# Optimization experiments

Measured on AMD Instinct MI355X. Metric: run time of the kernel, lower is better.

Reference implementation:

```python
import jax, jax.numpy as jnp
import numpy as np

D_MODEL = 1024
NUM_HEADS = 16


def setup_inputs() -> dict:
    key = jax.random.key(0)
    ks = jax.random.split(key, 5)
    B, S, D = 2, 2048, D_MODEL
    scale = 1.0 / np.sqrt(D)
    return {
        "x": jax.random.normal(ks[0], (B, S, D), dtype=jnp.float32),
        "q_proj_weight": jax.random.normal(ks[1], (D, D), dtype=jnp.float32) * scale,
        "k_proj_weight": jax.random.normal(ks[2], (D, D), dtype=jnp.float32) * scale,
        "v_proj_weight": jax.random.normal(ks[3], (D, D), dtype=jnp.float32) * scale,
        "o_proj_weight": jax.random.normal(ks[4], (D, D), dtype=jnp.float32) * scale,
    }


def _attn(x, qw, kw, vw, ow, num_heads):
    B, S, D = x.shape
    d_k = D // num_heads
    q = x @ qw.T  # [B,S,D]
    k = x @ kw.T
    v = x @ vw.T
    # split heads: [B, H, S, d_k]
    q = q.reshape(B, S, num_heads, d_k).transpose(0, 2, 1, 3)
    k = k.reshape(B, S, num_heads, d_k).transpose(0, 2, 1, 3)
    v = v.reshape(B, S, num_heads, d_k).transpose(0, 2, 1, 3)
    scores = jnp.einsum('bhqd,bhkd->bhqk', q, k) / jnp.sqrt(jnp.asarray(d_k, x.dtype))
    causal = jnp.tril(jnp.ones((S, S), dtype=bool))  # [S,S]
    scores = jnp.where(causal[None, None], scores, jnp.asarray(-jnp.inf, x.dtype))
    attn = jax.nn.softmax(scores, axis=-1)
    out = jnp.einsum('bhqk,bhkd->bhqd', attn, v)  # [B,H,S,d_k]
    out = out.transpose(0, 2, 1, 3).reshape(B, S, D)
    return out @ ow.T


def reference(x, q_proj_weight, k_proj_weight, v_proj_weight, o_proj_weight):
    return _attn(x, q_proj_weight, k_proj_weight, v_proj_weight, o_proj_weight, NUM_HEADS)
```

## Files before the change

### kernel.cpp

```cpp
#include <hip/hip_runtime.h>

typedef __attribute__((ext_vector_type(8))) short short8;
typedef __attribute__((ext_vector_type(4))) float f32x4;

#define MFMA(a,b,c) __builtin_amdgcn_mfma_f32_16x16x32_bf16((a),(b),(c),0,0,0)

#define B_  2
#define S_  2048
#define D_  1024
#define H_  16
#define DK  64
#define KDIM 1024

typedef unsigned int u32;
typedef __attribute__((address_space(1))) const u32 gu32;
typedef __attribute__((address_space(3))) u32 lu32;

__device__ __forceinline__ void gll16(const unsigned short* g, unsigned short* l){
  __builtin_amdgcn_global_load_lds((gu32*)g, (lu32*)l, 16, 0, 0);
}

__device__ __forceinline__ unsigned short f2bf(float f){
  unsigned int u = __float_as_uint(f);
  u += 0x7fffu + ((u >> 16) & 1u);
  return (unsigned short)(u >> 16);
}

__device__ __forceinline__ u32 pkbf(float lo, float hi){
  u32 a = __float_as_uint(lo) + 0x8000u;
  u32 b = __float_as_uint(hi) + 0x8000u;
  return __builtin_amdgcn_perm(b, a, 0x07060302u);
}

__global__ void cvt_all(const float* __restrict__ x,  const float* __restrict__ qw,
                        const float* __restrict__ kw, const float* __restrict__ vw,
                        const float* __restrict__ ow,
                        unsigned short* __restrict__ xb,  unsigned short* __restrict__ wqb,
                        unsigned short* __restrict__ wkb, unsigned short* __restrict__ wvb,
                        unsigned short* __restrict__ wob,
                        int n4x, int n4w){
  int i = blockIdx.x * 256 + threadIdx.x;
  const float* src; unsigned short* dst; int n4;
  switch (blockIdx.y) {
    case 0:  src = x;  dst = xb;  n4 = n4x; break;
    case 1:  src = qw; dst = wqb; n4 = n4w; break;
    case 2:  src = kw; dst = wkb; n4 = n4w; break;
    case 3:  src = vw; dst = wvb; n4 = n4w; break;
    default: src = ow; dst = wob; n4 = n4w; break;
  }
  if (i >= n4) return;
  float4 f = reinterpret_cast<const float4*>(src)[i];
  ushort4 u;
  u.x = f2bf(f.x); u.y = f2bf(f.y); u.z = f2bf(f.z); u.w = f2bf(f.w);
  reinterpret_cast<ushort4*>(dst)[i] = u;
}

__global__ __launch_bounds__(256) void gemm_qkv(
    const unsigned short* __restrict__ X,
    const unsigned short* __restrict__ Wq,
    const unsigned short* __restrict__ Wk,
    const unsigned short* __restrict__ Wv,
    unsigned short* __restrict__ Qo,
    unsigned short* __restrict__ Ko,
    unsigned short* __restrict__ Vo)
{
  const int z = blockIdx.z;
  const unsigned short* __restrict__ W = (z == 0) ? Wq : (z == 1) ? Wk : Wv;
  const int n0 = blockIdx.x * 64;
  const int m0 = blockIdx.y * 128;

  __shared__ unsigned short As0[128 * 32];
  __shared__ unsigned short As1[128 * 32];
  __shared__ unsigned short Bs0[64 * 32];
  __shared__ unsigned short Bs1[64 * 32];

  const int tid  = threadIdx.x;
  const int wid  = tid >> 6, lane = tid & 63;
  const int wm   = (wid >> 1) * 64, wn = (wid & 1) * 32;
  const int lr   = lane & 15, lk = (lane >> 4) * 8;

  const int srow = lane >> 2;
  const int scol = (lane & 3) * 8;
  const unsigned short* gA = X + (size_t)(m0 + wid * 32 + srow) * KDIM + scol;
  const unsigned short* gB = W + (size_t)(n0 + wid * 16 + srow) * KDIM + scol;
  unsigned short* lA0 = &As0[(wid * 32) * 32];
  unsigned short* lA1 = &As1[(wid * 32) * 32];
  unsigned short* lB0 = &Bs0[(wid * 16) * 32];
  unsigned short* lB1 = &Bs1[(wid * 16) * 32];

  f32x4 acc[4][2];
  const f32x4 z4 = {0.f, 0.f, 0.f, 0.f};
  for (int i = 0; i < 4; i++)
    for (int j = 0; j < 2; j++) acc[i][j] = z4;

  for (int k0 = 0; k0 < KDIM; k0 += 64) {
    __syncthreads();
    gll16(gA + k0,                  lA0);
    gll16(gA + 16 * KDIM + k0,      lA0 + 16 * 32);
    gll16(gA + k0 + 32,             lA1);
    gll16(gA + 16 * KDIM + k0 + 32, lA1 + 16 * 32);
    gll16(gB + k0,                  lB0);
    gll16(gB + k0 + 32,             lB1);
    __syncthreads();

    short8 a[4], b[2];
    for (int i = 0; i < 4; i++) a[i] = *(const short8*)&As0[(wm + i * 16 + lr) * 32 + lk];
    for (int j = 0; j < 2; j++) b[j] = *(const short8*)&Bs0[(wn + j * 16 + lr) * 32 + lk];
    if (z == 2) {
      for (int i = 0; i < 4; i++)
        for (int j = 0; j < 2; j++)
          acc[i][j] = MFMA(b[j], a[i], acc[i][j]);
    } else {
      for (int i = 0; i < 4; i++)
        for (int j = 0; j < 2; j++)
          acc[i][j] = MFMA(a[i], b[j], acc[i][j]);
    }
    for (int i = 0; i < 4; i++) a[i] = *(const short8*)&As1[(wm + i * 16 + lr) * 32 + lk];
    for (int j = 0; j < 2; j++) b[j] = *(const short8*)&Bs1[(wn + j * 16 + lr) * 32 + lk];
    if (z == 2) {
      for (int i = 0; i < 4; i++)
        for (int j = 0; j < 2; j++)
          acc[i][j] = MFMA(b[j], a[i], acc[i][j]);
    } else {
      for (int i = 0; i < 4; i++)
        for (int j = 0; j < 2; j++)
          acc[i][j] = MFMA(a[i], b[j], acc[i][j]);
    }
  }

  const int rbase = (lane >> 4) * 4;
  if (z == 2) {
    for (int i = 0; i < 4; i++)
      for (int j = 0; j < 2; j++)
        for (int r = 0; r < 4; r++) {
          int dfull = n0 + wn + j * 16 + rbase + r;
          int sfull = m0 + wm + i * 16 + lr;
          int h = dfull >> 6, d = dfull & 63;
          int bb = sfull >> 11, s = sfull & 2047;
          Vo[(((bb * H_ + h) * DK) + d) * S_ + s] = f2bf(acc[i][j][r]);
        }
  } else {
    for (int i = 0; i < 4; i++)
      for (int j = 0; j < 2; j++)
        for (int r = 0; r < 4; r++) {
          int m = m0 + wm + i * 16 + rbase + r;
          int n = n0 + wn + j * 16 + lr;
          float v = acc[i][j][r];
          int bb = m >> 11, s = m & 2047, h = n >> 6, d = n & 63;
          if (z == 0) {
            v *= 0.18033688f;
            Qo[(((bb * H_ + h) * S_) + s) * DK + d] = f2bf(v);
          } else {
            Ko[(((bb * H_ + h) * S_) + s) * DK + d] = f2bf(v);
          }
        }
  }
}

__global__ __launch_bounds__(512, 4) void attn(
    const unsigned short* __restrict__ Q,
    const unsigned short* __restrict__ K,
    const unsigned short* __restrict__ V,
    unsigned short* __restrict__ O)
{
  const int h = blockIdx.y, b = blockIdx.z;
  const int qt = b ? (15 - blockIdx.x) : blockIdx.x;

  const unsigned short* __restrict__ Qh = Q + (size_t)((b * H_ + h) * S_) * DK;
  const unsigned short* __restrict__ Kh = K + (size_t)((b * H_ + h) * S_) * DK;
  const unsigned short* __restrict__ Vh = V + (size_t)((b * H_ + h) * DK) * S_;

  __shared__ unsigned short Ks0[64 * 64];
  __shared__ unsigned short Ks1[64 * 64];
  __shared__ unsigned short Vs0[64 * 64];
  __shared__ unsigned short Vs1[64 * 64];
  __shared__ unsigned short Ps[8][16][72];

  const int tid = threadIdx.x, wid = tid >> 6, lane = tid & 63;
  const int lr = lane & 15;
  const int row4 = (lane >> 4) * 4;
  const int q0 = qt * 128;
  const int qcol = q0 + wid * 16 + lr;
  const int qwmin = q0 + wid * 16;
  const int qwmax = qwmin + 15;
  const int lk = (lane >> 4) * 8;

  const int pc0 = (((lane >> 4) + lr) & 7) * 8;
  const int pc1 = (((lane >> 4) + 4 + lr) & 7) * 8;

  const int sr8 = lane >> 3;
  const int sc8 = lane & 7;
  const int sg  = (sc8 - sr8) & 7;
  const int stRow = wid * 8 + sr8;
  const unsigned short* gK = Kh + (size_t)stRow * DK + sg * 8;
  const unsigned short* gV = Vh + (size_t)stRow * S_ + sg * 8;
  unsigned short* lK0 = &Ks0[wid * 8 * 64];
  unsigned short* lK1 = &Ks1[wid * 8 * 64];
  unsigned short* lV0 = &Vs0[wid * 8 * 64];
  unsigned short* lV1 = &Vs1[wid * 8 * 64];

  const short ONE = (short)0x3F80;
  const short8 ones = {ONE, ONE, ONE, ONE, ONE, ONE, ONE, ONE};

  short8 qf[2];
  qf[0] = *(const short8*)&Qh[(q0 + wid * 16 + lr) * DK + lk];
  qf[1] = *(const short8*)&Qh[(q0 + wid * 16 + lr) * DK + 32 + lk];

  const f32x4 z4 = {0.f, 0.f, 0.f, 0.f};
  f32x4 o[4];
  for (int i = 0; i < 4; i++) o[i] = z4;
  f32x4 rs = z4;

  auto tile = [&](int k0, const unsigned short* KS, const unsigned short* VS){
    if (k0 > qwmax) return;
    f32x4 sc[4];
    for (int nt = 0; nt < 4; nt++) {
      short8 kb0 = *(const short8*)&KS[(nt * 16 + lr) * 64 + pc0];
      short8 kb1 = *(const short8*)&KS[(nt * 16 + lr) * 64 + pc1];
      f32x4 s = MFMA(kb0, qf[0], z4);
      sc[nt] = MFMA(kb1, qf[1], s);
    }
    if (k0 + 63 > qwmin) {
      for (int nt = 0; nt < 4; nt++) {
        int kg = k0 + nt * 16 + row4;
        for (int r = 0; r < 4; r++)
          if (kg + r > qcol) sc[nt][r] = -INFINITY;
      }
    }
    for (int nt = 0; nt < 4; nt++) {
      float p0 = __builtin_amdgcn_exp2f(sc[nt][0]);
      float p1 = __builtin_amdgcn_exp2f(sc[nt][1]);
      float p2 = __builtin_amdgcn_exp2f(sc[nt][2]);
      float p3 = __builtin_amdgcn_exp2f(sc[nt][3]);
      uint2 pk;
      pk.x = pkbf(p0, p1);
      pk.y = pkbf(p2, p3);
      *(uint2*)&Ps[wid][lr][nt * 16 + row4] = pk;
    }
    short8 pf0 = *(const short8*)&Ps[wid][lr][lk];
    short8 pf1 = *(const short8*)&Ps[wid][lr][32 + lk];
    rs = MFMA(ones, pf0, rs);
    rs = MFMA(ones, pf1, rs);
    for (int dt = 0; dt < 4; dt++) {
      short8 vb0 = *(const short8*)&VS[(dt * 16 + lr) * 64 + pc0];
      short8 vb1 = *(const short8*)&VS[(dt * 16 + lr) * 64 + pc1];
      o[dt] = MFMA(vb0, pf0, o[dt]);
      o[dt] = MFMA(vb1, pf1, o[dt]);
    }
  };

  const int kt_end = 2 * qt + 2;

  gll16(gK, lK0);
  gll16(gV, lV0);

  for (int kt = 0; kt < kt_end; kt += 2) {
    const int k0 = kt * 64;
    __syncthreads();
    {
      gll16(gK + (size_t)(k0 + 64) * DK, lK1);
      gll16(gV + (k0 + 64),              lV1);
    }
    tile(k0, Ks0, Vs0);
    __syncthreads();
    if (kt + 2 < kt_end) {
      gll16(gK + (size_t)(k0 + 128) * DK, lK0);
      gll16(gV + (k0 + 128),              lV0);
    }
    tile(k0 + 64, Ks1, Vs1);
  }

  const float inv = 1.0f / rs[0];

  const int srow = q0 + wid * 16 + lr;
  for (int dt = 0; dt < 4; dt++) {
    uint2 pk;
    pk.x = pkbf(o[dt][0] * inv, o[dt][1] * inv);
    pk.y = pkbf(o[dt][2] * inv, o[dt][3] * inv);
    *(uint2*)&O[(size_t)(b * S_ + srow) * D_ + h * DK + dt * 16 + row4] = pk;
  }
}

__global__ __launch_bounds__(256) void gemm_oproj(
    const unsigned short* __restrict__ A,
    const unsigned short* __restrict__ W,
    float* __restrict__ out)
{
  const int n0 = blockIdx.x * 64;
  const int m0 = blockIdx.y * 128;

  __shared__ unsigned short As0[128 * 32];
  __shared__ unsigned short As1[128 * 32];
  __shared__ unsigned short Bs0[64 * 32];
  __shared__ unsigned short Bs1[64 * 32];

  const int tid  = threadIdx.x;
  const int wid  = tid >> 6, lane = tid & 63;
  const int wm   = (wid >> 1) * 64, wn = (wid & 1) * 32;
  const int lr   = lane & 15, lk = (lane >> 4) * 8;

  const int srow = lane >> 2;
  const int scol = (lane & 3) * 8;
  const unsigned short* gA = A + (size_t)(m0 + wid * 32 + srow) * KDIM + scol;
  const unsigned short* gB = W + (size_t)(n0 + wid * 16 + srow) * KDIM + scol;
  unsigned short* lA0 = &As0[(wid * 32) * 32];
  unsigned short* lA1 = &As1[(wid * 32) * 32];
  unsigned short* lB0 = &Bs0[(wid * 16) * 32];
  unsigned short* lB1 = &Bs1[(wid * 16) * 32];

  f32x4 acc[4][2];
  const f32x4 z4 = {0.f, 0.f, 0.f, 0.f};
  for (int i = 0; i < 4; i++)
    for (int j = 0; j < 2; j++) acc[i][j] = z4;

  for (int k0 = 0; k0 < KDIM; k0 += 64) {
    __syncthreads();
    gll16(gA + k0,                  lA0);
    gll16(gA + 16 * KDIM + k0,      lA0 + 16 * 32);
    gll16(gA + k0 + 32,             lA1);
    gll16(gA + 16 * KDIM + k0 + 32, lA1 + 16 * 32);
    gll16(gB + k0,                  lB0);
    gll16(gB + k0 + 32,             lB1);
    __syncthreads();

    short8 a[4], b[2];
    for (int i = 0; i < 4; i++) a[i] = *(const short8*)&As0[(wm + i * 16 + lr) * 32 + lk];
    for (int j = 0; j < 2; j++) b[j] = *(const short8*)&Bs0[(wn + j * 16 + lr) * 32 + lk];
    for (int i = 0; i < 4; i++)
      for (int j = 0; j < 2; j++)
        acc[i][j] = MFMA(a[i], b[j], acc[i][j]);
    for (int i = 0; i < 4; i++) a[i] = *(const short8*)&As1[(wm + i * 16 + lr) * 32 + lk];
    for (int j = 0; j < 2; j++) b[j] = *(const short8*)&Bs1[(wn + j * 16 + lr) * 32 + lk];
    for (int i = 0; i < 4; i++)
      for (int j = 0; j < 2; j++)
        acc[i][j] = MFMA(a[i], b[j], acc[i][j]);
  }

  const int rbase = (lane >> 4) * 4;
  for (int i = 0; i < 4; i++)
    for (int j = 0; j < 2; j++)
      for (int r = 0; r < 4; r++) {
        int m = m0 + wm + i * 16 + rbase + r;
        int n = n0 + wn + j * 16 + lr;
        out[(size_t)m * D_ + n] = acc[i][j][r];
      }
}

extern "C" void kernel_launch(void* const* d_in, const int* in_sizes, int n_in,
                              void* d_out, int out_size, void* d_ws, size_t ws_size,
                              hipStream_t stream) {
  const float* x  = (const float*)d_in[0];
  const float* qw = (const float*)d_in[1];
  const float* kw = (const float*)d_in[2];
  const float* vw = (const float*)d_in[3];
  const float* ow = (const float*)d_in[4];
  float* out = (float*)d_out;

  char* ws = (char*)d_ws;
  size_t off = 0;
  auto alloc = [&](size_t bytes) -> void* {
    void* p = ws + off;
    off += (bytes + 255) & ~(size_t)255;
    return p;
  };
  const size_t XN = (size_t)B_ * S_ * D_;
  const size_t WN = (size_t)D_ * D_;
  unsigned short* xb  = (unsigned short*)alloc(XN * 2);
  unsigned short* wqb = (unsigned short*)alloc(WN * 2);
  unsigned short* wkb = (unsigned short*)alloc(WN * 2);
  unsigned short* wvb = (unsigned short*)alloc(WN * 2);
  unsigned short* wob = (unsigned short*)alloc(WN * 2);
  unsigned short* Qb  = (unsigned short*)alloc(XN * 2);
  unsigned short* Kb  = (unsigned short*)alloc(XN * 2);
  unsigned short* Vb  = (unsigned short*)alloc(XN * 2);
  unsigned short* Ob  = (unsigned short*)alloc(XN * 2);

  cvt_all<<<dim3((XN / 4 + 255) / 256, 5), dim3(256), 0, stream>>>(
      x, qw, kw, vw, ow, xb, wqb, wkb, wvb, wob, (int)(XN / 4), (int)(WN / 4));

  gemm_qkv<<<dim3(D_ / 64, (B_ * S_) / 128, 3), dim3(256), 0, stream>>>(
      xb, wqb, wkb, wvb, Qb, Kb, Vb);

  attn<<<dim3(S_ / 128, H_, B_), dim3(512), 0, stream>>>(Qb, Kb, Vb, Ob);

  gemm_oproj<<<dim3(D_ / 64, (B_ * S_) / 128), dim3(256), 0, stream>>>(Ob, wob, out);
}
```

Before: 171.6 us.

## Enlarge GEMM tiles to 128x128 with XOR-swizzled 64-wide LDS layout

Both projection GEMMs move from 128x64 to 128x128 block tiles, so each wave computes a 64x64 sub-tile (4x4 MFMA accumulators) instead of 64x32. Each K-step of 64 is now stored as one 64-column LDS row with an XOR swizzle on the 16-byte chunk index, replacing the pair of 32-wide buffers, which is meant to avoid LDS bank conflicts. The goal is more MFMA work per LDS load and less global traffic per output. In exchange, accumulator registers double and there are half as many blocks, which may reduce occupancy.

```diff
diff --git a/kernel.cpp b/kernel.cpp
--- a/kernel.cpp
+++ b/kernel.cpp
@@ -66,64 +66,73 @@
 {
   const int z = blockIdx.z;
   const unsigned short* __restrict__ W = (z == 0) ? Wq : (z == 1) ? Wk : Wv;
-  const int n0 = blockIdx.x * 64;
+  const int n0 = blockIdx.x * 128;
   const int m0 = blockIdx.y * 128;
 
-  __shared__ unsigned short As0[128 * 32];
-  __shared__ unsigned short As1[128 * 32];
-  __shared__ unsigned short Bs0[64 * 32];
-  __shared__ unsigned short Bs1[64 * 32];
+  __shared__ unsigned short As[128 * 64];
+  __shared__ unsigned short Bs[128 * 64];
 
   const int tid  = threadIdx.x;
   const int wid  = tid >> 6, lane = tid & 63;
-  const int wm   = (wid >> 1) * 64, wn = (wid & 1) * 32;
-  const int lr   = lane & 15, lk = (lane >> 4) * 8;
-
-  const int srow = lane >> 2;
-  const int scol = (lane & 3) * 8;
+  const int wm   = (wid >> 1) * 64, wn = (wid & 1) * 64;
+  const int lr   = lane & 15, c = lane >> 4;
+  const int sw   = lr & 7;
+  const int pc0  = (c ^ sw) * 8;
+  const int pc1  = ((4 + c) ^ sw) * 8;
+
+  const int srow = lane >> 3;
+  const int scol = ((lane & 7) ^ srow) * 8;
   const unsigned short* gA = X + (size_t)(m0 + wid * 32 + srow) * KDIM + scol;
-  const unsigned short* gB = W + (size_t)(n0 + wid * 16 + srow) * KDIM + scol;
-  unsigned short* lA0 = &As0[(wid * 32) * 32];
-  unsigned short* lA1 = &As1[(wid * 32) * 32];
-  unsigned short* lB0 = &Bs0[(wid * 16) * 32];
-  unsigned short* lB1 = &Bs1[(wid * 16) * 32];
-
-  f32x4 acc[4][2];
+  const unsigned short* gB = W + (size_t)(n0 + wid * 32 + srow) * KDIM + scol;
+  unsigned short* lA = &As[(wid * 32) * 64];
+  unsigned short* lB = &Bs[(wid * 32) * 64];
+
+  f32x4 acc[4][4];
   const f32x4 z4 = {0.f, 0.f, 0.f, 0.f};
   for (int i = 0; i < 4; i++)
-    for (int j = 0; j < 2; j++) acc[i][j] = z4;
+    for (int j = 0; j < 4; j++) acc[i][j] = z4;
 
   for (int k0 = 0; k0 < KDIM; k0 += 64) {
     __syncthreads();
-    gll16(gA + k0,                  lA0);
-    gll16(gA + 16 * KDIM + k0,      lA0 + 16 * 32);
-    gll16(gA + k0 + 32,             lA1);
-    gll16(gA + 16 * KDIM + k0 + 32, lA1 + 16 * 32);
-    gll16(gB + k0,                  lB0);
-    gll16(gB + k0 + 32,             lB1);
-    __syncthreads();
-
-    short8 a[4], b[2];
-    for (int i = 0; i < 4; i++) a[i] = *(const short8*)&As0[(wm + i * 16 + lr) * 32 + lk];
-    for (int j = 0; j < 2; j++) b[j] = *(const short8*)&Bs0[(wn + j * 16 + lr) * 32 + lk];
+#pragma unroll
+    for (int i = 0; i < 4; i++) gll16(gA + (size_t)(i * 8) * KDIM + k0, lA + i * 512);
+#pragma unroll
+    for (int i = 0; i < 4; i++) gll16(gB + (size_t)(i * 8) * KDIM + k0, lB + i * 512);
+    __syncthreads();
+
+    short8 a[4], b[4];
+#pragma unroll
+    for (int i = 0; i < 4; i++) a[i] = *(const short8*)&As[(wm + i * 16 + lr) * 64 + pc0];
+#pragma unroll
+    for (int j = 0; j < 4; j++) b[j] = *(const short8*)&Bs[(wn + j * 16 + lr) * 64 + pc0];
     if (z == 2) {
+#pragma unroll
       for (int i = 0; i < 4; i++)
-        for (int j = 0; j < 2; j++)
+#pragma unroll
+        for (int j = 0; j < 4; j++)
           acc[i][j] = MFMA(b[j], a[i], acc[i][j]);
     } else {
+#pragma unroll
       for (int i = 0; i < 4; i++)
-        for (int j = 0; j < 2; j++)
+#pragma unroll
+        for (int j = 0; j < 4; j++)
           acc[i][j] = MFMA(a[i], b[j], acc[i][j]);
     }
-    for (int i = 0; i < 4; i++) a[i] = *(const short8*)&As1[(wm + i * 16 + lr) * 32 + lk];
-    for (int j = 0; j < 2; j++) b[j] = *(const short8*)&Bs1[(wn + j * 16 + lr) * 32 + lk];
+#pragma unroll
+    for (int i = 0; i < 4; i++) a[i] = *(const short8*)&As[(wm + i * 16 + lr) * 64 + pc1];
+#pragma unroll
+    for (int j = 0; j < 4; j++) b[j] = *(const short8*)&Bs[(wn + j * 16 + lr) * 64 + pc1];
     if (z == 2) {
+#pragma unroll
       for (int i = 0; i < 4; i++)
-        for (int j = 0; j < 2; j++)
+#pragma unroll
+        for (int j = 0; j < 4; j++)
           acc[i][j] = MFMA(b[j], a[i], acc[i][j]);
     } else {
+#pragma unroll
       for (int i = 0; i < 4; i++)
-        for (int j = 0; j < 2; j++)
+#pragma unroll
+        for (int j = 0; j < 4; j++)
           acc[i][j] = MFMA(a[i], b[j], acc[i][j]);
     }
   }
@@ -131,7 +140,7 @@
   const int rbase = (lane >> 4) * 4;
   if (z == 2) {
     for (int i = 0; i < 4; i++)
-      for (int j = 0; j < 2; j++)
+      for (int j = 0; j < 4; j++)
         for (int r = 0; r < 4; r++) {
           int dfull = n0 + wn + j * 16 + rbase + r;
           int sfull = m0 + wm + i * 16 + lr;
@@ -141,7 +150,7 @@
         }
   } else {
     for (int i = 0; i < 4; i++)
-      for (int j = 0; j < 2; j++)
+      for (int j = 0; j < 4; j++)
         for (int r = 0; r < 4; r++) {
           int m = m0 + wm + i * 16 + rbase + r;
           int n = n0 + wn + j * 16 + lr;
@@ -286,59 +295,64 @@
     const unsigned short* __restrict__ W,
     float* __restrict__ out)
 {
-  const int n0 = blockIdx.x * 64;
+  const int n0 = blockIdx.x * 128;
   const int m0 = blockIdx.y * 128;
 
-  __shared__ unsigned short As0[128 * 32];
-  __shared__ unsigned short As1[128 * 32];
-  __shared__ unsigned short Bs0[64 * 32];
-  __shared__ unsigned short Bs1[64 * 32];
+  __shared__ unsigned short As[128 * 64];
+  __shared__ unsigned short Bs[128 * 64];
 
   const int tid  = threadIdx.x;
   const int wid  = tid >> 6, lane = tid & 63;
-  const int wm   = (wid >> 1) * 64, wn = (wid & 1) * 32;
-  const int lr   = lane & 15, lk = (lane >> 4) * 8;
-
-  const int srow = lane >> 2;
-  const int scol = (lane & 3) * 8;
+  const int wm   = (wid >> 1) * 64, wn = (wid & 1) * 64;
+  const int lr   = lane & 15, c = lane >> 4;
+  const int sw   = lr & 7;
+  const int pc0  = (c ^ sw) * 8;
+  const int pc1  = ((4 + c) ^ sw) * 8;
+
+  const int srow = lane >> 3;
+  const int scol = ((lane & 7) ^ srow) * 8;
   const unsigned short* gA = A + (size_t)(m0 + wid * 32 + srow) * KDIM + scol;
-  const unsigned short* gB = W + (size_t)(n0 + wid * 16 + srow) * KDIM + scol;
-  unsigned short* lA0 = &As0[(wid * 32) * 32];
-  unsigned short* lA1 = &As1[(wid * 32) * 32];
-  unsigned short* lB0 = &Bs0[(wid * 16) * 32];
-  unsigned short* lB1 = &Bs1[(wid * 16) * 32];
-
-  f32x4 acc[4][2];
+  const unsigned short* gB = W + (size_t)(n0 + wid * 32 + srow) * KDIM + scol;
+  unsigned short* lA = &As[(wid * 32) * 64];
+  unsigned short* lB = &Bs[(wid * 32) * 64];
+
+  f32x4 acc[4][4];
   const f32x4 z4 = {0.f, 0.f, 0.f, 0.f};
   for (int i = 0; i < 4; i++)
-    for (int j = 0; j < 2; j++) acc[i][j] = z4;
+    for (int j = 0; j < 4; j++) acc[i][j] = z4;
 
   for (int k0 = 0; k0 < KDIM; k0 += 64) {
     __syncthreads();
-    gll16(gA + k0,                  lA0);
-    gll16(gA + 16 * KDIM + k0,      lA0 + 16 * 32);
-    gll16(gA + k0 + 32,             lA1);
-    gll16(gA + 16 * KDIM + k0 + 32, lA1 + 16 * 32);
-    gll16(gB + k0,                  lB0);
-    gll16(gB + k0 + 32,             lB1);
-    __syncthreads();
-
-    short8 a[4], b[2];
-    for (int i = 0; i < 4; i++) a[i] = *(const short8*)&As0[(wm + i * 16 + lr) * 32 + lk];
-    for (int j = 0; j < 2; j++) b[j] = *(const short8*)&Bs0[(wn + j * 16 + lr) * 32 + lk];
+#pragma unroll
+    for (int i = 0; i < 4; i++) gll16(gA + (size_t)(i * 8) * KDIM + k0, lA + i * 512);
+#pragma unroll
+    for (int i = 0; i < 4; i++) gll16(gB + (size_t)(i * 8) * KDIM + k0, lB + i * 512);
+    __syncthreads();
+
+    short8 a[4], b[4];
+#pragma unroll
+    for (int i = 0; i < 4; i++) a[i] = *(const short8*)&As[(wm + i * 16 + lr) * 64 + pc0];
+#pragma unroll
+    for (int j = 0; j < 4; j++) b[j] = *(const short8*)&Bs[(wn + j * 16 + lr) * 64 + pc0];
+#pragma unroll
     for (int i = 0; i < 4; i++)
-      for (int j = 0; j < 2; j++)
+#pragma unroll
+      for (int j = 0; j < 4; j++)
         acc[i][j] = MFMA(a[i], b[j], acc[i][j]);
-    for (int i = 0; i < 4; i++) a[i] = *(const short8*)&As1[(wm + i * 16 + lr) * 32 + lk];
-    for (int j = 0; j < 2; j++) b[j] = *(const short8*)&Bs1[(wn + j * 16 + lr) * 32 + lk];
+#pragma unroll
+    for (int i = 0; i < 4; i++) a[i] = *(const short8*)&As[(wm + i * 16 + lr) * 64 + pc1];
+#pragma unroll
+    for (int j = 0; j < 4; j++) b[j] = *(const short8*)&Bs[(wn + j * 16 + lr) * 64 + pc1];
+#pragma unroll
     for (int i = 0; i < 4; i++)
-      for (int j = 0; j < 2; j++)
+#pragma unroll
+      for (int j = 0; j < 4; j++)
         acc[i][j] = MFMA(a[i], b[j], acc[i][j]);
   }
 
   const int rbase = (lane >> 4) * 4;
   for (int i = 0; i < 4; i++)
-    for (int j = 0; j < 2; j++)
+    for (int j = 0; j < 4; j++)
       for (int r = 0; r < 4; r++) {
         int m = m0 + wm + i * 16 + rbase + r;
         int n = n0 + wn + j * 16 + lr;
@@ -378,10 +392,10 @@
   cvt_all<<<dim3((XN / 4 + 255) / 256, 5), dim3(256), 0, stream>>>(
       x, qw, kw, vw, ow, xb, wqb, wkb, wvb, wob, (int)(XN / 4), (int)(WN / 4));
 
-  gemm_qkv<<<dim3(D_ / 64, (B_ * S_) / 128, 3), dim3(256), 0, stream>>>(
+  gemm_qkv<<<dim3(D_ / 128, (B_ * S_) / 128, 3), dim3(256), 0, stream>>>(
       xb, wqb, wkb, wvb, Qb, Kb, Vb);
 
   attn<<<dim3(S_ / 128, H_, B_), dim3(512), 0, stream>>>(Qb, Kb, Vb, Ob);
 
-  gemm_oproj<<<dim3(D_ / 64, (B_ * S_) / 128), dim3(256), 0, stream>>>(Ob, wob, out);
-}
+  gemm_oproj<<<dim3(D_ / 128, (B_ * S_) / 128), dim3(256), 0, stream>>>(Ob, wob, out);
+}
```

New measurement: 177.2 us. 3.3% more time.
